# Kernel optimization log

Measured on AMD Instinct MI355X. Metric: run time of the kernel, lower is better.

## Reference

```python
import jax, jax.numpy as jnp
import numpy as np

B, N, D, H = 8, 128, 512, 8
HD = D // H
D2, D4 = D // 2, D // 4
E = 5
MAX_CD = 3.0
SPARSITY_RATIO = 0.3
K_TOP = max(1, int(N * (1.0 - SPARSITY_RATIO)))  # 89


def setup_inputs() -> dict:
    key = jax.random.key(0)
    ks = jax.random.split(key, 12)
    w = lambda k, s: jax.random.normal(k, s, jnp.float32) * 0.02
    return {
        'x': jax.random.normal(ks[0], (B, N, D), jnp.float32),
        'node_mask': jnp.ones((B, N), dtype=bool),
        'edge_features': jax.random.uniform(ks[1], (B, N, N, E), dtype=jnp.float32),
        'w_qkv': w(ks[2], (3 * D, D)),
        'w_proj': w(ks[3], (D, D)), 'b_proj': jnp.zeros((D,), jnp.float32),
        'w_np': w(ks[4], (D2, D)), 'b_np': jnp.zeros((D2,), jnp.float32),
        'w_ep': w(ks[5], (D4, D)), 'b_ep': jnp.zeros((D4,), jnp.float32),
        'w1': w(ks[6], (D2, D2 + D4 + 1)), 'b1': jnp.zeros((D2,), jnp.float32),
        'w2': w(ks[7], (D4, D2)), 'b2': jnp.zeros((D4,), jnp.float32),
        'w3': w(ks[8], (H, D4)), 'b3': jnp.zeros((H,), jnp.float32),
    }


def _chemical_distances(edge_features, node_mask):
    # bond_weights = {0: inf, 1: 1.0, 2: 0.8, 3: 0.6, 4: 0.9}
    table = jnp.array([jnp.inf, 1.0, 0.8, 0.6, 0.9], jnp.float32)
    strongest = jnp.argmax(edge_features, axis=-1)          # [B,N,N]
    wgt = table[strongest]
    pair_valid = node_mask[:, :, None] & node_mask[:, None, :]
    adj = jnp.where(pair_valid, wgt, jnp.inf)
    eye = jnp.eye(N, dtype=bool)
    adj = jnp.where(eye[None] & pair_valid, 0.0, adj)
    # Floyd-Warshall: masked nodes have inf rows/cols so plain FW == masked FW
    def body(Dm, kk):
        Dm = jnp.minimum(Dm, Dm[:, :, kk][:, :, None] + Dm[:, kk, :][:, None, :])
        return Dm, None
    Dm, _ = jax.lax.scan(body, adj, jnp.arange(N))
    return Dm, pair_valid


def reference(x, node_mask, edge_features, w_qkv, w_proj, b_proj,
              w_np, b_np, w_ep, b_ep, w1, b1, w2, b2, w3, b3):
    scale = HD ** -0.5
    qkv = (x @ w_qkv.T).reshape(B, N, 3, H, HD)
    q = jnp.moveaxis(qkv[:, :, 0], 2, 1)  # [B,H,N,hd]
    k = jnp.moveaxis(qkv[:, :, 1], 2, 1)
    v = jnp.moveaxis(qkv[:, :, 2], 2, 1)
    attn = jnp.einsum('bhqd,bhkd->bhqk', q * scale, k)

    # learned sparsity mask
    dist, pair_valid = _chemical_distances(edge_features, node_mask)
    node_proj = x @ w_np.T + b_np                                   # [B,N,D2]
    edge_feat = jnp.tanh(node_proj[:, :, None, :] + node_proj[:, None, :, :])  # [B,N,N,D2]
    # torch pads edge_feat with zeros to D before edge_feature_proj -> only first D2 cols matter
    edge_proj = edge_feat @ w_ep[:, :D2].T + b_ep                   # [B,N,N,D4]
    cd = jnp.clip(dist, 0.0, MAX_CD)
    combined = jnp.concatenate([edge_feat, edge_proj, (cd / MAX_CD)[..., None]], axis=-1)
    h1 = jax.nn.relu(combined @ w1.T + b1)
    h2 = jax.nn.relu(h1 @ w2.T + b2)
    probs = jax.nn.sigmoid(h2 @ w3.T + b3)                          # [B,N,N,H]
    sp = jnp.moveaxis(probs, -1, 1) * pair_valid[:, None].astype(jnp.float32)
    eye = jnp.eye(N, dtype=bool)
    sp = jnp.where(eye[None, None], 1.0, sp)                        # diagonal forced to 1

    # top-k sparsity on raw (masked) scores, then softmax over the sparse matrix
    masked = attn * sp
    vals, idx = jax.lax.top_k(masked, K_TOP)
    bi = jnp.arange(B)[:, None, None, None]
    hi = jnp.arange(H)[None, :, None, None]
    si = jnp.arange(N)[None, None, :, None]
    sparse = jnp.zeros_like(attn).at[bi, hi, si, idx].set(vals)
    aw = jax.nn.softmax(sparse, axis=-1)
    out = jnp.einsum('bhqk,bhkd->bhqd', aw, v)
    out = jnp.moveaxis(out, 1, 2).reshape(B, N, D)
    return out @ w_proj.T + b_proj
```

## Files before the change

### kernel.cpp

```cpp
#include <hip/hip_runtime.h>
#include <math.h>

#define Bb 8
#define Nn 128
#define Dd 512
#define Hh 8
#define KTOP 89

typedef short s16x8 __attribute__((ext_vector_type(8)));
typedef float f32x4 __attribute__((ext_vector_type(4)));

__device__ __forceinline__ unsigned short bf16r(float f) {
    unsigned int u = __float_as_uint(f);
    u += 0x7FFFu + ((u >> 16) & 1u);
    return (unsigned short)(u >> 16);
}
__device__ __forceinline__ float tanh_fast(float x) {
    x = fminf(fmaxf(x, -15.f), 15.f);
    float e = exp2f(x * 2.8853900817779268f);
    return (e - 1.f) / (e + 1.f);
}

__global__ __launch_bounds__(256)
void gemm_xwT(const float* __restrict__ A, const float* __restrict__ W,
              const float* __restrict__ bias, float* __restrict__ C,
              int M, int N, int K)
{
    __shared__ float As[16][64];
    __shared__ float Ws[16][64];
    const int tid = threadIdx.x;
    const int tx = tid & 15, ty = tid >> 4;
    const int m0 = blockIdx.x << 6, n0 = blockIdx.y << 6;
    const int lr = tid >> 2, lc = (tid & 3) << 2;
    float acc[4][4] = {};
    const float* Ap = A + (size_t)(m0 + lr) * K + lc;
    const float* Wp = W + (size_t)(n0 + lr) * K + lc;
    for (int k0 = 0; k0 < K; k0 += 16) {
        float4 a4 = *(const float4*)(Ap + k0);
        float4 w4 = *(const float4*)(Wp + k0);
        __syncthreads();
        As[lc+0][lr] = a4.x; As[lc+1][lr] = a4.y; As[lc+2][lr] = a4.z; As[lc+3][lr] = a4.w;
        Ws[lc+0][lr] = w4.x; Ws[lc+1][lr] = w4.y; Ws[lc+2][lr] = w4.z; Ws[lc+3][lr] = w4.w;
        __syncthreads();
#pragma unroll
        for (int kk = 0; kk < 16; ++kk) {
            float a[4], w[4];
            *(float4*)a = *(const float4*)&As[kk][tx << 2];
            *(float4*)w = *(const float4*)&Ws[kk][ty << 2];
#pragma unroll
            for (int i2 = 0; i2 < 4; ++i2)
#pragma unroll
                for (int j2 = 0; j2 < 4; ++j2)
                    acc[i2][j2] += a[i2] * w[j2];
        }
    }
#pragma unroll
    for (int i2 = 0; i2 < 4; ++i2) {
        const int m = m0 + (tx << 2) + i2;
#pragma unroll
        for (int j2 = 0; j2 < 4; ++j2) {
            const int n = n0 + (ty << 2) + j2;
            float v = acc[i2][j2];
            if (bias) v += bias[n];
            C[(size_t)m * N + n] = v;
        }
    }
}

__global__ __launch_bounds__(256)
void prep_fold(const float* __restrict__ w1, const float* __restrict__ wep,
               const float* __restrict__ b1, const float* __restrict__ bep,
               unsigned short* __restrict__ Afold, float* __restrict__ bc)
{
    const int n = blockIdx.x, k = threadIdx.x;
    const float* w1e = w1 + (size_t)n * 385 + 256;
    float acc = w1[(size_t)n * 385 + k];
#pragma unroll 4
    for (int m = 0; m < 128; ++m)
        acc += wep[(size_t)m * 512 + k] * w1e[m];
    Afold[(size_t)n * 256 + k] = bf16r(acc);
    if (k == 0) {
        float bacc = b1[n];
        for (int m = 0; m < 128; ++m) bacc += bep[m] * w1e[m];
        bc[n] = bacc;
    }
}

__global__ __launch_bounds__(256)
void prep2(const float* __restrict__ w1, const float* __restrict__ w2,
           const float* __restrict__ w3,
           float* __restrict__ w1last, unsigned short* __restrict__ w2b,
           unsigned short* __restrict__ w3b)
{
    const int t = blockIdx.x * 256 + threadIdx.x;
    if (t < 32768) w2b[t] = bf16r(w2[t]);
    if (t < 256) w1last[t] = w1[(size_t)t * 385 + 384];
    if (t < 2048) {
        const int o = t >> 7, k = t & 127;
        w3b[t] = (o < 8) ? bf16r(w3[o * 128 + k]) : (unsigned short)0;
    }
}

__global__ __launch_bounds__(256)
void build_adj(const float* __restrict__ efeat, float* __restrict__ adj)
{
    const int e = blockIdx.x * 256 + threadIdx.x;
    const int ii = (e >> 7) & 127, jj = e & 127;
    const float* p = efeat + (size_t)e * 5;
    float v0 = p[0], v1 = p[1], v2 = p[2], v3 = p[3], v4 = p[4];
    float best = v0; int bx = 0;
    if (v1 > best) { best = v1; bx = 1; }
    if (v2 > best) { best = v2; bx = 2; }
    if (v3 > best) { best = v3; bx = 3; }
    if (v4 > best) { best = v4; bx = 4; }
    float w = (bx == 1) ? 1.0f : (bx == 2) ? 0.8f : (bx == 3) ? 0.6f
            : (bx == 4) ? 0.9f : INFINITY;
    adj[e] = (ii == jj) ? 0.0f : w;
}

__global__ __launch_bounds__(256)
void minplus_square(const float* __restrict__ Din, float* __restrict__ Dout)
{
    __shared__ float Ds[128][132];
    const int tid = threadIdx.x;
    const int b = blockIdx.x >> 4;
    const int t = blockIdx.x & 15;
    const float* src = Din + (size_t)b * 16384;
    for (int e = tid; e < 16384; e += 256)
        Ds[e >> 7][e & 127] = src[e];
    __syncthreads();
    const int i  = (t << 3) + (tid >> 5);
    const int j0 = (tid & 31) << 2;
    float a0 = INFINITY, a1 = INFINITY, a2 = INFINITY, a3 = INFINITY;
#pragma unroll 4
    for (int k = 0; k < 128; ++k) {
        const float dik = Ds[i][k];
        float4 r = *(const float4*)&Ds[k][j0];
        a0 = fminf(a0, dik + r.x);
        a1 = fminf(a1, dik + r.y);
        a2 = fminf(a2, dik + r.z);
        a3 = fminf(a3, dik + r.w);
    }
    float4 o = {a0, a1, a2, a3};
    *(float4*)&Dout[(size_t)b * 16384 + i * 128 + j0] = o;
}

#define AS2 264
#define HS2 136

__global__ __launch_bounds__(512, 6)
void mlp3(const float* __restrict__ npf, const float* __restrict__ dist,
          const unsigned short* __restrict__ Afold, const float* __restrict__ bc,
          const float* __restrict__ w1last,
          const unsigned short* __restrict__ w2b, const float* __restrict__ b2,
          const unsigned short* __restrict__ w3b, const float* __restrict__ b3,
          float* __restrict__ sp)
{
    const int bid = blockIdx.x;
    const int jh = bid & 1;
    const int i  = (bid >> 1) & 127;
    const int b  = bid >> 8;
    const int j0 = jh << 6;
    const int tid = threadIdx.x;
    const int w  = tid >> 6;
    const int l  = tid & 63;
    const int lr = l & 15;
    const int lq = l >> 4;

    __shared__ unsigned short A1s[64 * AS2];
    __shared__ unsigned short Hs[64 * HS2];
    __shared__ float npis[256];
    __shared__ float cdl[64];

    if (tid < 256) npis[tid] = npf[(size_t)(b * Nn + i) * 256 + tid];
    else if (tid < 320) {
        const int r = tid - 256;
        float dv = dist[((size_t)(b * Nn) + i) * Nn + j0 + r];
        cdl[r] = fminf(dv, 3.0f) * (1.0f / 3.0f);
    }
    __syncthreads();

    {
        const int row = tid & 63;
        const int c0  = (tid >> 6) * 32;
        const float* npj = npf + (size_t)(b * Nn + j0 + row) * 256 + c0;
#pragma unroll
        for (int c = 0; c < 32; c += 8) {
            float4 x0 = *(const float4*)(npj + c);
            float4 x1 = *(const float4*)(npj + c + 4);
            float v[8] = {x0.x, x0.y, x0.z, x0.w, x1.x, x1.y, x1.z, x1.w};
            unsigned int pk[4];
#pragma unroll
            for (int e = 0; e < 8; e += 2) {
                float t0 = tanh_fast(npis[c0 + c + e]     + v[e]);
                float t1 = tanh_fast(npis[c0 + c + e + 1] + v[e + 1]);
                pk[e >> 1] = ((unsigned int)bf16r(t1) << 16) | bf16r(t0);
            }
            *(uint4*)&A1s[row * AS2 + c0 + c] = *(uint4*)pk;
        }
    }
    __syncthreads();

    f32x4 acc2[4] = {};
    for (int p = 0; p < 2; ++p) {
        const int nc = p * 128 + w * 16;
        f32x4 acc[4] = {};
        for (int k0 = 0; k0 < 256; k0 += 32) {
            s16x8 bw = *(const s16x8*)&Afold[(size_t)(nc + lr) * 256 + k0 + lq * 8];
#pragma unroll
            for (int mt = 0; mt < 4; ++mt) {
                s16x8 av = *(const s16x8*)&A1s[(mt * 16 + lr) * AS2 + k0 + lq * 8];
                acc[mt] = __builtin_amdgcn_mfma_f32_16x16x32_bf16(av, bw, acc[mt], 0, 0, 0);
            }
        }
        const float wl = w1last[nc + lr];
        const float bb = bc[nc + lr];
#pragma unroll
        for (int mt = 0; mt < 4; ++mt) {
            f32x4 cdv = *(const f32x4*)&cdl[mt * 16 + lq * 4];
#pragma unroll
            for (int rg = 0; rg < 4; ++rg) {
                float hv = fmaxf(acc[mt][rg] + cdv[rg] * wl + bb, 0.f);
                Hs[(mt * 16 + lq * 4 + rg) * HS2 + w * 16 + lr] = bf16r(hv);
            }
        }
        __syncthreads();
        for (int k0 = 0; k0 < 128; k0 += 32) {
            s16x8 bw = *(const s16x8*)&w2b[(size_t)(w * 16 + lr) * 256 + p * 128 + k0 + lq * 8];
#pragma unroll
            for (int mt = 0; mt < 4; ++mt) {
                s16x8 av = *(const s16x8*)&Hs[(mt * 16 + lr) * HS2 + k0 + lq * 8];
                acc2[mt] = __builtin_amdgcn_mfma_f32_16x16x32_bf16(av, bw, acc2[mt], 0, 0, 0);
            }
        }
        __syncthreads();
    }

    {
        const float bb = b2[w * 16 + lr];
#pragma unroll
        for (int mt = 0; mt < 4; ++mt)
#pragma unroll
            for (int rg = 0; rg < 4; ++rg)
                Hs[(mt * 16 + lq * 4 + rg) * HS2 + w * 16 + lr] =
                    bf16r(fmaxf(acc2[mt][rg] + bb, 0.f));
    }
    __syncthreads();

    if (w < 4) {
        f32x4 acc3 = {};
        for (int k0 = 0; k0 < 128; k0 += 32) {
            s16x8 bw = *(const s16x8*)&w3b[lr * 128 + k0 + lq * 8];
            s16x8 av = *(const s16x8*)&Hs[(w * 16 + lr) * HS2 + k0 + lq * 8];
            acc3 = __builtin_amdgcn_mfma_f32_16x16x32_bf16(av, bw, acc3, 0, 0, 0);
        }
        if (lr < 8) {
            const float bb = b3[lr];
            const int jbase = j0 + w * 16 + lq * 4;
            float pv[4];
#pragma unroll
            for (int rg = 0; rg < 4; ++rg) {
                float lg = acc3[rg] + bb;
                float s  = 1.0f / (1.0f + exp2f(-lg * 1.4426950408889634f));
                pv[rg] = (jbase + rg == i) ? 1.0f : s;
            }
            *(float4*)&sp[(((size_t)(b * Hh + lr)) * Nn + i) * Nn + jbase] = *(float4*)pv;
        }
    }
}

__global__ __launch_bounds__(256)
void attn_kernel(const float* __restrict__ qkv, const float* __restrict__ sp,
                 float* __restrict__ aout)
{
    const int blk = blockIdx.x;
    const int qt = blk & 15;
    const int h  = (blk >> 4) & 7;
    const int b  = blk >> 7;
    const int tid = threadIdx.x;
    const int w = tid >> 6, lane = tid & 63;

    __shared__ float kT[64][132];
    __shared__ float sw[4][128];
    __shared__ float qs[4][64];

    {
        const int j = tid >> 1, d0 = (tid & 1) << 5;
        const float* kp = qkv + (size_t)(b * Nn + j) * 1536 + 512 + h * 64 + d0;
#pragma unroll
        for (int c = 0; c < 32; c += 4) {
            float4 kv = *(const float4*)(kp + c);
            kT[d0+c+0][j] = kv.x;
            kT[d0+c+1][j] = kv.y;
            kT[d0+c+2][j] = kv.z;
            kT[d0+c+3][j] = kv.w;
        }
    }
    __syncthreads();

    const float* vbase = qkv + (size_t)(b * Nn) * 1536 + 1024 + h * 64 + lane;

    for (int r = 0; r < 2; ++r) {
        const int q = (qt << 3) + (w << 1) + r;
        qs[w][lane] = qkv[(size_t)(b * Nn + q) * 1536 + h * 64 + lane];
        float acc1 = 0.f, acc2 = 0.f;
#pragma unroll
        for (int d = 0; d < 64; d += 4) {
            float qv[4];
            *(float4*)qv = *(const float4*)&qs[w][d];
            acc1 += qv[0]*kT[d+0][lane]    + qv[1]*kT[d+1][lane]
                  + qv[2]*kT[d+2][lane]    + qv[3]*kT[d+3][lane];
            acc2 += qv[0]*kT[d+0][lane+64] + qv[1]*kT[d+1][lane+64]
                  + qv[2]*kT[d+2][lane+64] + qv[3]*kT[d+3][lane+64];
        }
        const float* sprow = sp + (((size_t)(b * Hh + h)) * Nn + q) * Nn;
        const float m1 = acc1 * 0.125f * sprow[lane];
        const float m2 = acc2 * 0.125f * sprow[lane + 64];
        sw[w][lane]      = m1;
        sw[w][lane + 64] = m2;
        int r1 = 0, r2 = 0;
        for (int jj = 0; jj < 128; ++jj) {
            const float mv = sw[w][jj];
            r1 += (mv > m1 || (mv == m1 && jj < lane)) ? 1 : 0;
            r2 += (mv > m2 || (mv == m2 && jj < lane + 64)) ? 1 : 0;
        }
        float gm = fmaxf(m1, m2);
#pragma unroll
        for (int off = 32; off > 0; off >>= 1) gm = fmaxf(gm, __shfl_xor(gm, off, 64));
        const float M = fmaxf(gm, 0.0f);
        const float e1 = expf((r1 < KTOP ? m1 : 0.0f) - M);
        const float e2 = expf((r2 < KTOP ? m2 : 0.0f) - M);
        float dsum = e1 + e2;
#pragma unroll
        for (int off = 32; off > 0; off >>= 1) dsum += __shfl_xor(dsum, off, 64);
        const float inv = 1.0f / dsum;
        sw[w][lane]      = e1 * inv;
        sw[w][lane + 64] = e2 * inv;
        float acc = 0.f;
        for (int jj = 0; jj < 128; ++jj)
            acc += sw[w][jj] * vbase[(size_t)jj * 1536];
        aout[(size_t)(b * Nn + q) * Dd + h * 64 + lane] = acc;
    }
}

extern "C" void kernel_launch(void* const* d_in, const int* in_sizes, int n_in,
                              void* d_out, int out_size, void* d_ws, size_t ws_size,
                              hipStream_t stream)
{
    const float* x      = (const float*)d_in[0];
    const float* efeat  = (const float*)d_in[2];
    const float* w_qkv  = (const float*)d_in[3];
    const float* w_proj = (const float*)d_in[4];
    const float* b_proj = (const float*)d_in[5];
    const float* w_np   = (const float*)d_in[6];
    const float* b_np   = (const float*)d_in[7];
    const float* w_ep   = (const float*)d_in[8];
    const float* b_ep   = (const float*)d_in[9];
    const float* w1     = (const float*)d_in[10];
    const float* b1     = (const float*)d_in[11];
    const float* w2     = (const float*)d_in[12];
    const float* b2     = (const float*)d_in[13];
    const float* w3     = (const float*)d_in[14];
    const float* b3     = (const float*)d_in[15];
    float* out = (float*)d_out;

    float* ws     = (float*)d_ws;
    float* qkv    = ws;
    float* npb    = qkv    + 1572864;
    float* dist   = npb    + 262144;
    float* spb    = dist   + 131072;
    float* aout   = spb    + 1048576;
    float* w1last = aout   + 524288;
    float* bc     = w1last + 256;
    unsigned short* Afold = (unsigned short*)(bc + 256);
    unsigned short* w2b   = Afold + 65536;
    unsigned short* w3b   = w2b   + 32768;
    float* dtmp   = (float*)(w3b + 2048);

    prep_fold<<<256, 256, 0, stream>>>(w1, w_ep, b1, b_ep, Afold, bc);
    prep2<<<128, 256, 0, stream>>>(w1, w2, w3, w1last, w2b, w3b);
    gemm_xwT<<<dim3(16, 24), 256, 0, stream>>>(x, w_qkv, nullptr, qkv, 1024, 1536, 512);
    gemm_xwT<<<dim3(16, 4),  256, 0, stream>>>(x, w_np, b_np, npb, 1024, 256, 512);
    build_adj<<<512, 256, 0, stream>>>(efeat, dist);
    minplus_square<<<128, 256, 0, stream>>>(dist, dtmp);
    minplus_square<<<128, 256, 0, stream>>>(dtmp, dist);
    mlp3<<<2048, 512, 0, stream>>>(npb, dist, Afold, bc, w1last, w2b, b2, w3b, b3, spb);
    attn_kernel<<<1024, 256, 0, stream>>>(qkv, spb, aout);
    gemm_xwT<<<dim3(16, 8),  256, 0, stream>>>(aout, w_proj, b_proj, out, 1024, 512, 512);
}
```

Measured before the change: 328.1 us.

## Merge prep kernels into one launch and make mlp3 a persistent grid

Folds prep_fold, prep2 and build_adj into a single prep_all kernel that picks its work by block index, which removes two kernel launches. mlp3 now runs a fixed grid of 768 blocks that loop over the 2048 tiles, sized to keep all blocks resident at once. Several inner MFMA loops get explicit unroll pragmas. Tiles are still spread unevenly over the blocks, and the extra unrolling may raise register pressure.

```diff
diff --git a/kernel.cpp b/kernel.cpp
--- a/kernel.cpp
+++ b/kernel.cpp
@@ -68,54 +68,50 @@
 }
 
 __global__ __launch_bounds__(256)
-void prep_fold(const float* __restrict__ w1, const float* __restrict__ wep,
-               const float* __restrict__ b1, const float* __restrict__ bep,
-               unsigned short* __restrict__ Afold, float* __restrict__ bc)
-{
-    const int n = blockIdx.x, k = threadIdx.x;
-    const float* w1e = w1 + (size_t)n * 385 + 256;
-    float acc = w1[(size_t)n * 385 + k];
+void prep_all(const float* __restrict__ w1, const float* __restrict__ wep,
+              const float* __restrict__ b1, const float* __restrict__ bep,
+              const float* __restrict__ w2, const float* __restrict__ w3,
+              const float* __restrict__ efeat,
+              unsigned short* __restrict__ Afold, float* __restrict__ bc,
+              float* __restrict__ w1last, unsigned short* __restrict__ w2b,
+              unsigned short* __restrict__ w3b, float* __restrict__ adj)
+{
+    const int blk = blockIdx.x;
+    if (blk < 256) {
+        const int n = blk, k = threadIdx.x;
+        const float* w1e = w1 + (size_t)n * 385 + 256;
+        float acc = w1[(size_t)n * 385 + k];
 #pragma unroll 4
-    for (int m = 0; m < 128; ++m)
-        acc += wep[(size_t)m * 512 + k] * w1e[m];
-    Afold[(size_t)n * 256 + k] = bf16r(acc);
-    if (k == 0) {
-        float bacc = b1[n];
-        for (int m = 0; m < 128; ++m) bacc += bep[m] * w1e[m];
-        bc[n] = bacc;
-    }
-}
-
-__global__ __launch_bounds__(256)
-void prep2(const float* __restrict__ w1, const float* __restrict__ w2,
-           const float* __restrict__ w3,
-           float* __restrict__ w1last, unsigned short* __restrict__ w2b,
-           unsigned short* __restrict__ w3b)
-{
-    const int t = blockIdx.x * 256 + threadIdx.x;
-    if (t < 32768) w2b[t] = bf16r(w2[t]);
-    if (t < 256) w1last[t] = w1[(size_t)t * 385 + 384];
-    if (t < 2048) {
-        const int o = t >> 7, k = t & 127;
-        w3b[t] = (o < 8) ? bf16r(w3[o * 128 + k]) : (unsigned short)0;
-    }
-}
-
-__global__ __launch_bounds__(256)
-void build_adj(const float* __restrict__ efeat, float* __restrict__ adj)
-{
-    const int e = blockIdx.x * 256 + threadIdx.x;
-    const int ii = (e >> 7) & 127, jj = e & 127;
-    const float* p = efeat + (size_t)e * 5;
-    float v0 = p[0], v1 = p[1], v2 = p[2], v3 = p[3], v4 = p[4];
-    float best = v0; int bx = 0;
-    if (v1 > best) { best = v1; bx = 1; }
-    if (v2 > best) { best = v2; bx = 2; }
-    if (v3 > best) { best = v3; bx = 3; }
-    if (v4 > best) { best = v4; bx = 4; }
-    float w = (bx == 1) ? 1.0f : (bx == 2) ? 0.8f : (bx == 3) ? 0.6f
-            : (bx == 4) ? 0.9f : INFINITY;
-    adj[e] = (ii == jj) ? 0.0f : w;
+        for (int m = 0; m < 128; ++m)
+            acc += wep[(size_t)m * 512 + k] * w1e[m];
+        Afold[(size_t)n * 256 + k] = bf16r(acc);
+        if (k == 0) {
+            float bacc = b1[n];
+            for (int m = 0; m < 128; ++m) bacc += bep[m] * w1e[m];
+            bc[n] = bacc;
+        }
+    } else if (blk < 384) {
+        const int t = (blk - 256) * 256 + threadIdx.x;
+        if (t < 32768) w2b[t] = bf16r(w2[t]);
+        if (t < 256) w1last[t] = w1[(size_t)t * 385 + 384];
+        if (t < 2048) {
+            const int o = t >> 7, k = t & 127;
+            w3b[t] = (o < 8) ? bf16r(w3[o * 128 + k]) : (unsigned short)0;
+        }
+    } else {
+        const int e = (blk - 384) * 256 + threadIdx.x;
+        const int ii = (e >> 7) & 127, jj = e & 127;
+        const float* p = efeat + (size_t)e * 5;
+        float v0 = p[0], v1 = p[1], v2 = p[2], v3 = p[3], v4 = p[4];
+        float best = v0; int bx = 0;
+        if (v1 > best) { best = v1; bx = 1; }
+        if (v2 > best) { best = v2; bx = 2; }
+        if (v3 > best) { best = v3; bx = 3; }
+        if (v4 > best) { best = v4; bx = 4; }
+        float w = (bx == 1) ? 1.0f : (bx == 2) ? 0.8f : (bx == 3) ? 0.6f
+                : (bx == 4) ? 0.9f : INFINITY;
+        adj[e] = (ii == jj) ? 0.0f : w;
+    }
 }
 
 __global__ __launch_bounds__(256)
@@ -147,6 +143,7 @@
 
 #define AS2 264
 #define HS2 136
+#define MLP_GRID 768
 
 __global__ __launch_bounds__(512, 6)
 void mlp3(const float* __restrict__ npf, const float* __restrict__ dist,
@@ -156,11 +153,6 @@
           const unsigned short* __restrict__ w3b, const float* __restrict__ b3,
           float* __restrict__ sp)
 {
-    const int bid = blockIdx.x;
-    const int jh = bid & 1;
-    const int i  = (bid >> 1) & 127;
-    const int b  = bid >> 8;
-    const int j0 = jh << 6;
     const int tid = threadIdx.x;
     const int w  = tid >> 6;
     const int l  = tid & 63;
@@ -172,6 +164,12 @@
     __shared__ float npis[256];
     __shared__ float cdl[64];
 
+    for (int bid = blockIdx.x; bid < 2048; bid += MLP_GRID) {
+    const int jh = bid & 1;
+    const int i  = (bid >> 1) & 127;
+    const int b  = bid >> 8;
+    const int j0 = jh << 6;
+
     if (tid < 256) npis[tid] = npf[(size_t)(b * Nn + i) * 256 + tid];
     else if (tid < 320) {
         const int r = tid - 256;
@@ -202,9 +200,11 @@
     __syncthreads();
 
     f32x4 acc2[4] = {};
+#pragma unroll
     for (int p = 0; p < 2; ++p) {
         const int nc = p * 128 + w * 16;
         f32x4 acc[4] = {};
+#pragma unroll
         for (int k0 = 0; k0 < 256; k0 += 32) {
             s16x8 bw = *(const s16x8*)&Afold[(size_t)(nc + lr) * 256 + k0 + lq * 8];
 #pragma unroll
@@ -225,6 +225,7 @@
             }
         }
         __syncthreads();
+#pragma unroll
         for (int k0 = 0; k0 < 128; k0 += 32) {
             s16x8 bw = *(const s16x8*)&w2b[(size_t)(w * 16 + lr) * 256 + p * 128 + k0 + lq * 8];
 #pragma unroll
@@ -249,6 +250,7 @@
 
     if (w < 4) {
         f32x4 acc3 = {};
+#pragma unroll
         for (int k0 = 0; k0 < 128; k0 += 32) {
             s16x8 bw = *(const s16x8*)&w3b[lr * 128 + k0 + lq * 8];
             s16x8 av = *(const s16x8*)&Hs[(w * 16 + lr) * HS2 + k0 + lq * 8];
@@ -266,6 +268,7 @@
             }
             *(float4*)&sp[(((size_t)(b * Hh + lr)) * Nn + i) * Nn + jbase] = *(float4*)pv;
         }
+    }
     }
 }
 
@@ -377,14 +380,13 @@
     unsigned short* w3b   = w2b   + 32768;
     float* dtmp   = (float*)(w3b + 2048);
 
-    prep_fold<<<256, 256, 0, stream>>>(w1, w_ep, b1, b_ep, Afold, bc);
-    prep2<<<128, 256, 0, stream>>>(w1, w2, w3, w1last, w2b, w3b);
+    prep_all<<<896, 256, 0, stream>>>(w1, w_ep, b1, b_ep, w2, w3, efeat,
+                                      Afold, bc, w1last, w2b, w3b, dist);
     gemm_xwT<<<dim3(16, 24), 256, 0, stream>>>(x, w_qkv, nullptr, qkv, 1024, 1536, 512);
     gemm_xwT<<<dim3(16, 4),  256, 0, stream>>>(x, w_np, b_np, npb, 1024, 256, 512);
-    build_adj<<<512, 256, 0, stream>>>(efeat, dist);
     minplus_square<<<128, 256, 0, stream>>>(dist, dtmp);
     minplus_square<<<128, 256, 0, stream>>>(dtmp, dist);
-    mlp3<<<2048, 512, 0, stream>>>(npb, dist, Afold, bc, w1last, w2b, b2, w3b, b3, spb);
+    mlp3<<<MLP_GRID, 512, 0, stream>>>(npb, dist, Afold, bc, w1last, w2b, b2, w3b, b3, spb);
     attn_kernel<<<1024, 256, 0, stream>>>(qkv, spb, aout);
     gemm_xwT<<<dim3(16, 8),  256, 0, stream>>>(aout, w_proj, b_proj, out, 1024, 512, 512);
 }
```

After: 358.2 us. 1.09x slower.
